# Kernel optimization log

Hardware: AMD Instinct MI355X
Metric: run time of the kernel (lower is better)

The kernel has to match this reference:

```python
import jax, jax.numpy as jnp
import numpy as np

DECAY = 0.99
EPS = 1e-05
N, K, D = 32768, 8192, 64


def setup_inputs() -> dict:
    key = jax.random.key(0)
    k1, k2, k3 = jax.random.split(key, 3)
    return {
        "inputs": jax.random.normal(k1, (N, D), dtype=jnp.float32),
        "embedding_w": jax.random.normal(k2, (K, D), dtype=jnp.float32),
        "ema_w": jax.random.normal(k3, (K, D), dtype=jnp.float32),
        "ema_cluster_size": jnp.zeros((K,), dtype=jnp.float32),
    }


def reference(inputs, embedding_w, ema_w, ema_cluster_size):
    k = embedding_w.shape[0]
    # pairwise squared L2 distances: [N, K]
    distances = (
        jnp.sum(inputs ** 2, axis=1, keepdims=True)
        + jnp.sum(embedding_w ** 2, axis=1)
        - 2.0 * inputs @ embedding_w.T
    )
    encoding_indices = jnp.argmin(distances, axis=1)           # [N] int
    encodings = jax.nn.one_hot(encoding_indices, k, dtype=inputs.dtype)  # [N, K]
    codebook = embedding_w  # returned codebook is the PRE-update weight (as in torch source)

    # EMA updates (training branch), expressed functionally
    cluster_size = ema_cluster_size * DECAY + (1.0 - DECAY) * jnp.sum(encodings, axis=0)
    n = jnp.sum(cluster_size)
    cluster_size = (cluster_size + EPS) / (n + k * EPS) * n
    dw = encodings.T @ inputs                                   # [K, D]
    ema_w_new = ema_w * DECAY + (1.0 - DECAY) * dw
    embedding_new = ema_w_new / cluster_size[:, None]

    return (encodings, codebook, cluster_size, ema_w_new, embedding_new)
```

## Files before the change

### kernel.cpp

```cpp
#include <hip/hip_runtime.h>
#include <hip/hip_bf16.h>

#define N_PTS 32768
#define K_CLU 8192
#define D_DIM 64
#define DECAYF 0.99f
#define OMDF   0.01f
#define EPSF   1e-5f

typedef _Float16 v8h __attribute__((ext_vector_type(8)));
typedef float    v4f __attribute__((ext_vector_type(4)));

#define OFF_COUNTS 0
#define OFF_DW     (32768)
#define OFF_NSUM   (OFF_DW + 2097152)
#define OFF_EHI    (OFF_NSUM + 16)
#define OFF_ELO    (OFF_EHI + 1048576)
#define OFF_E2     (OFF_ELO + 1048576)

__global__ __launch_bounds__(256) void vq_prep(
    const float* __restrict__ emb, const float* __restrict__ ema_cs,
    _Float16* __restrict__ ehi, _Float16* __restrict__ elo,
    float* __restrict__ e2, float* __restrict__ nsum)
{
    const int wave = threadIdx.x >> 6;
    const int lane = threadIdx.x & 63;
    if (blockIdx.x < 2048) {
        const int row = blockIdx.x * 4 + wave;
        float v = emb[(size_t)row * D_DIM + lane];
        _Float16 h = (_Float16)v;
        _Float16 l = (_Float16)(v - (float)h);
        ehi[(size_t)row * D_DIM + lane] = h;
        elo[(size_t)row * D_DIM + lane] = l;
        float s = v * v;
        #pragma unroll
        for (int m = 1; m < 64; m <<= 1) s += __shfl_xor(s, m, 64);
        if (lane == 0) e2[row] = s;
    } else {
        const int t = (blockIdx.x - 2048) * 256 + threadIdx.x;
        float v = ema_cs[t];
        #pragma unroll
        for (int m = 1; m < 64; m <<= 1) v += __shfl_xor(v, m, 64);
        if (lane == 0) atomicAdd(nsum, v);
    }
}

__global__ __launch_bounds__(256) void vq_fused(
    const float* __restrict__ x,
    const _Float16* __restrict__ ehi, const _Float16* __restrict__ elo,
    const float* __restrict__ e2,
    float* __restrict__ enc,
    unsigned int* __restrict__ counts,
    float* __restrict__ dw)
{
    __shared__ _Float16 sEhi[128 * 72];
    __shared__ _Float16 sElo[128 * 72];
    __shared__ float    sE2[128];

    const int bid  = blockIdx.x;
    const int tid  = threadIdx.x;
    const int lane = tid & 63;
    const int quad = lane >> 4;
    const int l15  = lane & 15;
    const int ptbase = bid * 64 + (tid >> 6) * 16;

    v8h xh[2], xl[2];
    {
        const int pt = ptbase + l15;
        const float* xp = x + (size_t)pt * D_DIM + quad * 8;
        #pragma unroll
        for (int c = 0; c < 2; ++c) {
            float4 a = *(const float4*)(xp + c * 32);
            float4 b = *(const float4*)(xp + c * 32 + 4);
            float vv[8] = {a.x, a.y, a.z, a.w, b.x, b.y, b.z, b.w};
            v8h hh, ll;
            #pragma unroll
            for (int j = 0; j < 8; ++j) {
                _Float16 h = (_Float16)vv[j];
                hh[j] = h;
                ll[j] = (_Float16)(vv[j] - (float)h);
            }
            xh[c] = hh; xl[c] = ll;
        }
    }

    float best[4]; int bidx4[4];
    #pragma unroll
    for (int i = 0; i < 4; ++i) { best[i] = 3.4e38f; bidx4[i] = 0; }

    v4f* enc4 = (v4f*)enc;
    const size_t zbase = (size_t)bid * 131072 + tid;
    const v4f zz = {0.f, 0.f, 0.f, 0.f};

    for (int chunk = 0; chunk < 64; ++chunk) {
        const int kbase = chunk * 128;
        __syncthreads();
        {
            const uint4* gh = (const uint4*)(ehi + (size_t)kbase * D_DIM);
            const uint4* gl = (const uint4*)(elo + (size_t)kbase * D_DIM);
            #pragma unroll
            for (int it = 0; it < 4; ++it) {
                int u = tid + 256 * it;
                int row = u >> 3, uc = u & 7;
                *(uint4*)&sEhi[row * 72 + uc * 8] = gh[row * 8 + uc];
                *(uint4*)&sElo[row * 72 + uc * 8] = gl[row * 8 + uc];
            }
            if (tid < 128) sE2[tid] = e2[kbase + tid];
        }
        __syncthreads();

        const size_t zo = zbase + (size_t)chunk * 2048;
        #pragma unroll
        for (int sub = 0; sub < 8; ++sub) {
            __builtin_nontemporal_store(zz, enc4 + zo + sub * 256);

            const int nl = sub * 16 + l15;
            v8h bh0 = *(const v8h*)&sEhi[nl * 72 + quad * 8];
            v8h bh1 = *(const v8h*)&sEhi[nl * 72 + 32 + quad * 8];
            v8h bl0 = *(const v8h*)&sElo[nl * 72 + quad * 8];
            v8h bl1 = *(const v8h*)&sElo[nl * 72 + 32 + quad * 8];
            const float e2v = sE2[nl];
            const int kidx = kbase + nl;
            v4f acc = {0.f, 0.f, 0.f, 0.f};
            acc = __builtin_amdgcn_mfma_f32_16x16x32_f16(xh[0], bh0, acc, 0, 0, 0);
            acc = __builtin_amdgcn_mfma_f32_16x16x32_f16(xh[1], bh1, acc, 0, 0, 0);
            acc = __builtin_amdgcn_mfma_f32_16x16x32_f16(xl[0], bh0, acc, 0, 0, 0);
            acc = __builtin_amdgcn_mfma_f32_16x16x32_f16(xl[1], bh1, acc, 0, 0, 0);
            acc = __builtin_amdgcn_mfma_f32_16x16x32_f16(xh[0], bl0, acc, 0, 0, 0);
            acc = __builtin_amdgcn_mfma_f32_16x16x32_f16(xh[1], bl1, acc, 0, 0, 0);
            #pragma unroll
            for (int r = 0; r < 4; ++r) {
                float dist = fmaf(acc[r], -2.0f, e2v);
                if (dist < best[r]) { best[r] = dist; bidx4[r] = kidx; }
            }
        }
    }

    #pragma unroll
    for (int i = 0; i < 4; ++i) {
        #pragma unroll
        for (int m = 1; m < 16; m <<= 1) {
            float ov = __shfl_xor(best[i], m, 64);
            int   oi = __shfl_xor(bidx4[i], m, 64);
            if (ov < best[i] || (ov == best[i] && oi < bidx4[i])) { best[i] = ov; bidx4[i] = oi; }
        }
    }

    __syncthreads();

    if (l15 == 0) {
        #pragma unroll
        for (int r = 0; r < 4; ++r) {
            int p = ptbase + quad * 4 + r;
            enc[(size_t)p * K_CLU + bidx4[r]] = 1.0f;
            atomicAdd(&counts[bidx4[r]], 1u);
        }
    }

    #pragma unroll
    for (int j = 0; j < 16; ++j) {
        const int src = (j >> 2) * 16;
        const int r = j & 3;
        int k = __shfl(bidx4[r], src, 64);
        float val = x[(size_t)(ptbase + j) * D_DIM + lane];
        atomicAdd(&dw[(size_t)k * D_DIM + lane], val);
    }
}

__global__ __launch_bounds__(256) void vq_finalize(
    const float* __restrict__ emb, const float* __restrict__ ema_w,
    const float* __restrict__ ema_cs,
    const unsigned int* __restrict__ counts, const float* __restrict__ dw,
    const float* __restrict__ nsum,
    float* __restrict__ out)
{
    const size_t ENC = (size_t)N_PTS * K_CLU;
    float* out_codebook = out + ENC;
    float* out_cs       = out_codebook + (size_t)K_CLU * D_DIM;
    float* out_ema      = out_cs + K_CLU;
    float* out_emb      = out_ema + (size_t)K_CLU * D_DIM;

    const int gid = blockIdx.x * 256 + threadIdx.x;
    const int k = gid >> 6, d = gid & 63;
    float dwv = dw[gid];
    float en  = DECAYF * ema_w[gid] + OMDF * dwv;
    float cnt = (float)counts[k];
    float cs_raw = DECAYF * ema_cs[k] + OMDF * cnt;
    float n  = DECAYF * nsum[0] + OMDF * (float)N_PTS;
    float cs = (cs_raw + EPSF) / (n + (float)K_CLU * EPSF) * n;
    out_codebook[gid] = emb[gid];
    out_ema[gid] = en;
    out_emb[gid] = en / cs;
    if (d == 0) out_cs[k] = cs;
}

extern "C" void kernel_launch(void* const* d_in, const int* in_sizes, int n_in,
                              void* d_out, int out_size, void* d_ws, size_t ws_size,
                              hipStream_t stream)
{
    const float* x      = (const float*)d_in[0];
    const float* emb    = (const float*)d_in[1];
    const float* ema_w  = (const float*)d_in[2];
    const float* ema_cs = (const float*)d_in[3];
    float* out = (float*)d_out;
    char* ws = (char*)d_ws;

    unsigned int* counts = (unsigned int*)(ws + OFF_COUNTS);
    float*        dw     = (float*)(ws + OFF_DW);
    float*        nsum   = (float*)(ws + OFF_NSUM);
    _Float16*     ehi    = (_Float16*)(ws + OFF_EHI);
    _Float16*     elo    = (_Float16*)(ws + OFF_ELO);
    float*        e2     = (float*)(ws + OFF_E2);

    hipMemsetAsync(ws + OFF_COUNTS, 0, (OFF_NSUM + 16) - OFF_COUNTS, stream);

    vq_prep<<<2080, 256, 0, stream>>>(emb, ema_cs, ehi, elo, e2, nsum);
    vq_fused<<<512, 256, 0, stream>>>(x, ehi, elo, e2, out, counts, dw);
    vq_finalize<<<2048, 256, 0, stream>>>(emb, ema_w, ema_cs, counts, dw, nsum, out);
}
```

Measured before the change: 1.079 ms.

## Double-buffer codebook tiles via direct global-to-LDS loads with XOR swizzle

Codebook hi/lo fp16 tiles are now staged into two LDS buffers with global_load_lds, prefetching the next chunk while the current one is computed. This removes one barrier per chunk and the register round-trip of the old loads. The padded LDS rows are replaced by an XOR swizzle applied when the prep kernel writes the layout, to avoid bank conflicts without padding. The MFMA chain is also split into two independent accumulators to shorten the dependency chain, which slightly changes the summation order of the dot product.

```diff
diff --git a/kernel.cpp b/kernel.cpp
--- a/kernel.cpp
+++ b/kernel.cpp
@@ -10,6 +10,9 @@
 
 typedef _Float16 v8h __attribute__((ext_vector_type(8)));
 typedef float    v4f __attribute__((ext_vector_type(4)));
+
+#define AS1 __attribute__((address_space(1)))
+#define AS3 __attribute__((address_space(3)))
 
 #define OFF_COUNTS 0
 #define OFF_DW     (32768)
@@ -30,8 +33,9 @@
         float v = emb[(size_t)row * D_DIM + lane];
         _Float16 h = (_Float16)v;
         _Float16 l = (_Float16)(v - (float)h);
-        ehi[(size_t)row * D_DIM + lane] = h;
-        elo[(size_t)row * D_DIM + lane] = l;
+        const int sw = (lane & 7) | ((((lane >> 3) ^ (row & 7)) & 7) << 3);
+        ehi[(size_t)row * D_DIM + sw] = h;
+        elo[(size_t)row * D_DIM + sw] = l;
         float s = v * v;
         #pragma unroll
         for (int m = 1; m < 64; m <<= 1) s += __shfl_xor(s, m, 64);
@@ -53,16 +57,17 @@
     unsigned int* __restrict__ counts,
     float* __restrict__ dw)
 {
-    __shared__ _Float16 sEhi[128 * 72];
-    __shared__ _Float16 sElo[128 * 72];
-    __shared__ float    sE2[128];
+    __shared__ _Float16 sEhi[2][128 * 64];
+    __shared__ _Float16 sElo[2][128 * 64];
+    __shared__ float    sE2[2][128];
 
     const int bid  = blockIdx.x;
     const int tid  = threadIdx.x;
+    const int wave = tid >> 6;
     const int lane = tid & 63;
     const int quad = lane >> 4;
     const int l15  = lane & 15;
-    const int ptbase = bid * 64 + (tid >> 6) * 16;
+    const int ptbase = bid * 64 + wave * 16;
 
     v8h xh[2], xl[2];
     {
@@ -92,48 +97,69 @@
     const size_t zbase = (size_t)bid * 131072 + tid;
     const v4f zz = {0.f, 0.f, 0.f, 0.f};
 
+    auto stage = [&](int b, int chunk) {
+        const size_t gb = (size_t)chunk * 128 * 128;
+        const char* gh = (const char*)ehi + gb;
+        const char* gl = (const char*)elo + gb;
+        char* lh = (char*)&sEhi[b][0];
+        char* ll = (char*)&sElo[b][0];
+        #pragma unroll
+        for (int i = 0; i < 4; ++i) {
+            const int off = wave * 4096 + i * 1024;
+            __builtin_amdgcn_global_load_lds(
+                (const AS1 void*)(gh + off + lane * 16), (AS3 void*)(lh + off), 16, 0, 0);
+            __builtin_amdgcn_global_load_lds(
+                (const AS1 void*)(gl + off + lane * 16), (AS3 void*)(ll + off), 16, 0, 0);
+        }
+        if (wave == 0) {
+            const char* ge = (const char*)(e2 + (size_t)chunk * 128);
+            char* le = (char*)&sE2[b][0];
+            #pragma unroll
+            for (int i = 0; i < 2; ++i) {
+                __builtin_amdgcn_global_load_lds(
+                    (const AS1 void*)(ge + i * 256 + lane * 4), (AS3 void*)(le + i * 256), 4, 0, 0);
+            }
+        }
+    };
+
+    stage(0, 0);
+    __syncthreads();
+
     for (int chunk = 0; chunk < 64; ++chunk) {
+        const int cur = chunk & 1;
+        if (chunk + 1 < 64) stage(cur ^ 1, chunk + 1);
+
         const int kbase = chunk * 128;
-        __syncthreads();
-        {
-            const uint4* gh = (const uint4*)(ehi + (size_t)kbase * D_DIM);
-            const uint4* gl = (const uint4*)(elo + (size_t)kbase * D_DIM);
-            #pragma unroll
-            for (int it = 0; it < 4; ++it) {
-                int u = tid + 256 * it;
-                int row = u >> 3, uc = u & 7;
-                *(uint4*)&sEhi[row * 72 + uc * 8] = gh[row * 8 + uc];
-                *(uint4*)&sElo[row * 72 + uc * 8] = gl[row * 8 + uc];
-            }
-            if (tid < 128) sE2[tid] = e2[kbase + tid];
-        }
-        __syncthreads();
-
         const size_t zo = zbase + (size_t)chunk * 2048;
         #pragma unroll
         for (int sub = 0; sub < 8; ++sub) {
             __builtin_nontemporal_store(zz, enc4 + zo + sub * 256);
 
             const int nl = sub * 16 + l15;
-            v8h bh0 = *(const v8h*)&sEhi[nl * 72 + quad * 8];
-            v8h bh1 = *(const v8h*)&sEhi[nl * 72 + 32 + quad * 8];
-            v8h bl0 = *(const v8h*)&sElo[nl * 72 + quad * 8];
-            v8h bl1 = *(const v8h*)&sElo[nl * 72 + 32 + quad * 8];
-            const float e2v = sE2[nl];
+            const int ro = nl * 64;
+            const int swz = (nl & 7) << 3;
+            v8h bh0 = *(const v8h*)&sEhi[cur][ro + ((quad << 3) ^ swz)];
+            v8h bh1 = *(const v8h*)&sEhi[cur][ro + (((4 + quad) << 3) ^ swz)];
+            v8h bl0 = *(const v8h*)&sElo[cur][ro + ((quad << 3) ^ swz)];
+            v8h bl1 = *(const v8h*)&sElo[cur][ro + (((4 + quad) << 3) ^ swz)];
+            const float e2v = sE2[cur][nl];
             const int kidx = kbase + nl;
-            v4f acc = {0.f, 0.f, 0.f, 0.f};
-            acc = __builtin_amdgcn_mfma_f32_16x16x32_f16(xh[0], bh0, acc, 0, 0, 0);
-            acc = __builtin_amdgcn_mfma_f32_16x16x32_f16(xh[1], bh1, acc, 0, 0, 0);
-            acc = __builtin_amdgcn_mfma_f32_16x16x32_f16(xl[0], bh0, acc, 0, 0, 0);
-            acc = __builtin_amdgcn_mfma_f32_16x16x32_f16(xl[1], bh1, acc, 0, 0, 0);
-            acc = __builtin_amdgcn_mfma_f32_16x16x32_f16(xh[0], bl0, acc, 0, 0, 0);
-            acc = __builtin_amdgcn_mfma_f32_16x16x32_f16(xh[1], bl1, acc, 0, 0, 0);
+            v4f acc0 = {0.f, 0.f, 0.f, 0.f};
+            v4f acc1 = {0.f, 0.f, 0.f, 0.f};
+            acc0 = __builtin_amdgcn_mfma_f32_16x16x32_f16(xh[0], bh0, acc0, 0, 0, 0);
+            acc1 = __builtin_amdgcn_mfma_f32_16x16x32_f16(xh[1], bh1, acc1, 0, 0, 0);
+            acc0 = __builtin_amdgcn_mfma_f32_16x16x32_f16(xl[0], bh0, acc0, 0, 0, 0);
+            acc1 = __builtin_amdgcn_mfma_f32_16x16x32_f16(xl[1], bh1, acc1, 0, 0, 0);
+            acc0 = __builtin_amdgcn_mfma_f32_16x16x32_f16(xh[0], bl0, acc0, 0, 0, 0);
+            acc1 = __builtin_amdgcn_mfma_f32_16x16x32_f16(xh[1], bl1, acc1, 0, 0, 0);
             #pragma unroll
             for (int r = 0; r < 4; ++r) {
-                float dist = fmaf(acc[r], -2.0f, e2v);
+                float dot = acc0[r] + acc1[r];
+                float dist = fmaf(dot, -2.0f, e2v);
                 if (dist < best[r]) { best[r] = dist; bidx4[r] = kidx; }
             }
         }
+        __syncthreads();
     }
 
     #pragma unroll
```

New measurement: 1.068 ms. About the same (-1.0%).
